# Optimization experiments

Hardware: AMD Instinct MI355X
Metric: run time of the kernel (lower is better)

## Reference

```python
import jax, jax.numpy as jnp
import numpy as np

B, T, L, F = 32, 512, 16, 128   # utterances, max frames, frame-spec width, specgram_height
H = 128                          # hidden_size1 == hidden_size2
C = 61                           # TIMIT phoneme count


def _p(key, shape, scale):
    return jax.random.normal(key, shape, jnp.float32) * scale


def setup_inputs() -> dict:
    key = jax.random.key(0)
    ks = jax.random.split(key, 32)
    s = 1.0 / np.sqrt(H)
    inp = {}
    inp["x"] = jax.random.normal(ks[0], (B, T, L, F), jnp.float32)
    inp["lengths"] = jax.random.randint(ks[1], (B,), T // 2, T + 1, jnp.int32)
    i = 2
    # rnn1: tanh-RNN, 2 layers, bidirectional (layer0 in=F, layer1 in=2H); dir axis 0
    for name, din in (("r1l0", F), ("r1l1", 2 * H)):
        inp[name + "_Wih"] = _p(ks[i], (2, H, din), s); i += 1
        inp[name + "_Whh"] = _p(ks[i], (2, H, H), s); i += 1
        inp[name + "_bih"] = _p(ks[i], (2, H), s); i += 1
        inp[name + "_bhh"] = _p(ks[i], (2, H), s); i += 1
    # rnn2: GRU, 2 layers, bidirectional (in=2H for both layers); gates packed r,z,n
    for name in ("g0", "g1"):
        inp[name + "_Wih"] = _p(ks[i], (2, 3 * H, 2 * H), s); i += 1
        inp[name + "_Whh"] = _p(ks[i], (2, 3 * H, H), s); i += 1
        inp[name + "_bih"] = _p(ks[i], (2, 3 * H), s); i += 1
        inp[name + "_bhh"] = _p(ks[i], (2, 3 * H), s); i += 1
    inp["fc_W"] = _p(ks[i], (C, 2 * H), s); i += 1
    inp["fc_b"] = _p(ks[i], (C,), s)
    return inp


def _rnn_bidir(x, Wih, Whh, bih, bhh):
    # x: (N, S, din) -> (N, S, 2H); PyTorch nn.RNN(tanh), bidirectional
    outs = []
    for d in range(2):
        xw = jnp.einsum('bli,hi->blh', x, Wih[d]) + bih[d]
        W, b = Whh[d], bhh[d]
        def step(h, xt):
            h = jnp.tanh(xt + h @ W.T + b)
            return h, h
        h0 = jnp.zeros((x.shape[0], W.shape[0]), x.dtype)
        _, ys = jax.lax.scan(step, h0, jnp.swapaxes(xw, 0, 1), reverse=(d == 1))
        outs.append(jnp.swapaxes(ys, 0, 1))
    return jnp.concatenate(outs, -1)


def _gru_bidir(x, Wih, Whh, bih, bhh):
    # x: (N, S, din) -> (N, S, 2H); PyTorch nn.GRU, bidirectional
    outs = []
    for d in range(2):
        xw = jnp.einsum('bli,hi->blh', x, Wih[d]) + bih[d]  # (N, S, 3H)
        W, b = Whh[d], bhh[d]
        def step(h, xt):
            g = h @ W.T + b
            xr, xz, xn = jnp.split(xt, 3, -1)
            gr, gz, gn = jnp.split(g, 3, -1)
            r = jax.nn.sigmoid(xr + gr)
            z = jax.nn.sigmoid(xz + gz)
            n = jnp.tanh(xn + r * gn)
            h = (1.0 - z) * n + z * h
            return h, h
        h0 = jnp.zeros((x.shape[0], W.shape[1]), x.dtype)
        _, ys = jax.lax.scan(step, h0, jnp.swapaxes(xw, 0, 1), reverse=(d == 1))
        outs.append(jnp.swapaxes(ys, 0, 1))
    return jnp.concatenate(outs, -1)


def reference(x, lengths,
              r1l0_Wih, r1l0_Whh, r1l0_bih, r1l0_bhh,
              r1l1_Wih, r1l1_Whh, r1l1_bih, r1l1_bhh,
              g0_Wih, g0_Whh, g0_bih, g0_bhh,
              g1_Wih, g1_Whh, g1_bih, g1_bhh,
              fc_W, fc_b):
    b, t, l, f = x.shape
    # per-sample rnn1 loop == one batched pass over all B*T frames (eval mode: no dropout)
    o = _rnn_bidir(x.reshape(b * t, l, f), r1l0_Wih, r1l0_Whh, r1l0_bih, r1l0_bhh)
    o = _rnn_bidir(o, r1l1_Wih, r1l1_Whh, r1l1_bih, r1l1_bhh)
    o = o[:, -1, :].reshape(b, t, 2 * H)       # last inner timestep per frame
    o = _gru_bidir(o, g0_Wih, g0_Whh, g0_bih, g0_bhh)
    o = _gru_bidir(o, g1_Wih, g1_Whh, g1_bih, g1_bhh)
    logits = o @ fc_W.T + fc_b                  # (B, T, C)
    mask = jnp.arange(t)[None, :] < lengths[:, None]
    # ragged scatter: concat first lengths[i] timesteps of each sample
    return logits.reshape(b * t, -1)[mask.reshape(-1)]
```

## Files before the change

### kernel.cpp

```cpp
#include <hip/hip_runtime.h>
#include <hip/hip_bf16.h>

#define B_ 32
#define T_ 512
#define L_ 16
#define F_ 128
#define H_ 128
#define C_ 61
#define NF_ (B_*T_)
#define CH_ 4096

typedef unsigned int u32;
typedef unsigned short u16;
typedef __attribute__((ext_vector_type(8))) short s16x8;
typedef __attribute__((ext_vector_type(4))) float f32x4;

__device__ __forceinline__ float bflo(u32 v){ return __uint_as_float(v << 16); }
__device__ __forceinline__ float bfhi(u32 v){ return __uint_as_float(v & 0xffff0000u); }
__device__ __forceinline__ u16 f2bf(float f){
  u32 u = __float_as_uint(f);
  u += 0x7fffu + ((u >> 16) & 1u);
  return (u16)(u >> 16);
}
__device__ __forceinline__ u32 pack2(float a, float b){
  return (u32)f2bf(a) | ((u32)f2bf(b) << 16);
}
__device__ __forceinline__ float fast_tanh(float x){
  float e = __expf(2.f*x);
  return 1.f - 2.f*__builtin_amdgcn_rcpf(e + 1.f);
}
__device__ __forceinline__ float fast_sigmoid(float x){
  return __builtin_amdgcn_rcpf(1.f + __expf(-x));
}
__device__ __forceinline__ f32x4 mfma16(s16x8 a, s16x8 b, f32x4 c){
  return __builtin_amdgcn_mfma_f32_16x16x32_bf16(a, b, c, 0, 0, 0);
}
__device__ __forceinline__ s16x8 packfrag(const float* p){
  const float4 a = *(const float4*)p;
  const float4 b = *(const float4*)(p+4);
  union { s16x8 v; u32 w[4]; } f;
  f.w[0]=pack2(a.x,a.y); f.w[1]=pack2(a.z,a.w);
  f.w[2]=pack2(b.x,b.y); f.w[3]=pack2(b.z,b.w);
  return f.v;
}

__global__ __launch_bounds__(256) void l0_mfma(
    const float* __restrict__ x,
    const float* __restrict__ Wih,
    const float* __restrict__ Whh,
    const float* __restrict__ bih,
    const float* __restrict__ bhh,
    u16* __restrict__ out)
{
  __shared__ __align__(16) u16 Hb[2][32][136];
  __shared__ __align__(16) u16 Xb[2][32][136];
  const int t = threadIdx.x;
  const int lane = t & 63, wv = t >> 6;
  const int l15 = lane & 15, kg = lane >> 4;
  const int dir = blockIdx.y;
  const int f0 = blockIdx.x * 32;
  s16x8 wih[2][4], whh[2][4];
  {
    const float* Wid = Wih + dir*16384;
    const float* Whd = Whh + dir*16384;
    #pragma unroll
    for (int nt = 0; nt < 2; nt++){
      const int u = wv*32 + nt*16 + l15;
      #pragma unroll
      for (int kc = 0; kc < 4; kc++){
        const int k = kc*32 + kg*8;
        wih[nt][kc] = packfrag(&Wid[u*128 + k]);
        whh[nt][kc] = packfrag(&Whd[u*128 + k]);
      }
    }
  }
  float bv[2];
  bv[0] = bih[dir*128 + wv*32 + l15]      + bhh[dir*128 + wv*32 + l15];
  bv[1] = bih[dir*128 + wv*32 + 16 + l15] + bhh[dir*128 + wv*32 + 16 + l15];
  const int sr = t >> 3, sc = (t & 7) * 16;
  {
    *(uint4*)&Hb[0][sr][sc]   = make_uint4(0,0,0,0);
    *(uint4*)&Hb[0][sr][sc+8] = make_uint4(0,0,0,0);
    const int s0 = dir ? 15 : 0;
    const float4* xp = (const float4*)&x[(size_t)(f0+sr)*2048 + s0*128 + sc];
    const float4 v0 = xp[0], v1 = xp[1], v2 = xp[2], v3 = xp[3];
    *(uint4*)&Xb[0][sr][sc]   = make_uint4(pack2(v0.x,v0.y),pack2(v0.z,v0.w),
                                           pack2(v1.x,v1.y),pack2(v1.z,v1.w));
    *(uint4*)&Xb[0][sr][sc+8] = make_uint4(pack2(v2.x,v2.y),pack2(v2.z,v2.w),
                                           pack2(v3.x,v3.y),pack2(v3.z,v3.w));
  }
  __syncthreads();
  int cur = 0;
  for (int st = 0; st < 16; st++){
    const int s = dir ? (15-st) : st;
    float4 p0,p1,p2,p3;
    if (st < 15){
      const int sn = dir ? (14-st) : (st+1);
      const float4* xp = (const float4*)&x[(size_t)(f0+sr)*2048 + sn*128 + sc];
      p0 = xp[0]; p1 = xp[1]; p2 = xp[2]; p3 = xp[3];
    }
    f32x4 acc00 = {0.f,0.f,0.f,0.f}, acc01 = acc00, acc10 = acc00, acc11 = acc00;
    #pragma unroll
    for (int kc = 0; kc < 4; kc++){
      const int ko = kc*32 + kg*8;
      const s16x8 ax0 = *(const s16x8*)&Xb[cur][l15][ko];
      const s16x8 ax1 = *(const s16x8*)&Xb[cur][16+l15][ko];
      const s16x8 ah0 = *(const s16x8*)&Hb[cur][l15][ko];
      const s16x8 ah1 = *(const s16x8*)&Hb[cur][16+l15][ko];
      acc00 = mfma16(ax0, wih[0][kc], acc00);
      acc01 = mfma16(ax0, wih[1][kc], acc01);
      acc10 = mfma16(ax1, wih[0][kc], acc10);
      acc11 = mfma16(ax1, wih[1][kc], acc11);
      acc00 = mfma16(ah0, whh[0][kc], acc00);
      acc01 = mfma16(ah0, whh[1][kc], acc01);
      acc10 = mfma16(ah1, whh[0][kc], acc10);
      acc11 = mfma16(ah1, whh[1][kc], acc11);
    }
    const int u0 = wv*32 + l15, u1 = wv*32 + 16 + l15;
    u16* op = out + (size_t)f0*4096 + s*256 + dir*128;
    #pragma unroll
    for (int r = 0; r < 4; r++){
      const int m0r = kg*4 + r, m1r = 16 + kg*4 + r;
      u16 h00 = f2bf(fast_tanh(acc00[r] + bv[0]));
      u16 h01 = f2bf(fast_tanh(acc01[r] + bv[1]));
      u16 h10 = f2bf(fast_tanh(acc10[r] + bv[0]));
      u16 h11 = f2bf(fast_tanh(acc11[r] + bv[1]));
      Hb[cur^1][m0r][u0] = h00;
      Hb[cur^1][m0r][u1] = h01;
      Hb[cur^1][m1r][u0] = h10;
      Hb[cur^1][m1r][u1] = h11;
      op[(size_t)m0r*4096 + u0] = h00;
      op[(size_t)m0r*4096 + u1] = h01;
      op[(size_t)m1r*4096 + u0] = h10;
      op[(size_t)m1r*4096 + u1] = h11;
    }
    if (st < 15){
      *(uint4*)&Xb[cur^1][sr][sc]   = make_uint4(pack2(p0.x,p0.y),pack2(p0.z,p0.w),
                                                 pack2(p1.x,p1.y),pack2(p1.z,p1.w));
      *(uint4*)&Xb[cur^1][sr][sc+8] = make_uint4(pack2(p2.x,p2.y),pack2(p2.z,p2.w),
                                                 pack2(p3.x,p3.y),pack2(p3.z,p3.w));
    }
    __syncthreads();
    cur ^= 1;
  }
}

__global__ __launch_bounds__(256) void l1f_mfma(
    const u16* __restrict__ U,
    const float* __restrict__ Wih,
    const float* __restrict__ Whh,
    const float* __restrict__ bih,
    const float* __restrict__ bhh,
    u16* __restrict__ out)
{
  __shared__ __align__(16) u16 Hb[2][32][136];
  __shared__ __align__(16) u16 Xb[2][32][264];
  const int t = threadIdx.x;
  const int lane = t & 63, wv = t >> 6;
  const int l15 = lane & 15, kg = lane >> 4;
  const int f0 = blockIdx.x * 32;
  s16x8 wih[2][8], whh[2][4];
  {
    #pragma unroll
    for (int nt = 0; nt < 2; nt++){
      const int u = wv*32 + nt*16 + l15;
      #pragma unroll
      for (int kc = 0; kc < 8; kc++)
        wih[nt][kc] = packfrag(&Wih[u*256 + kc*32 + kg*8]);
      #pragma unroll
      for (int kc = 0; kc < 4; kc++)
        whh[nt][kc] = packfrag(&Whh[u*128 + kc*32 + kg*8]);
    }
  }
  float bv[2];
  bv[0] = bih[wv*32 + l15]      + bhh[wv*32 + l15];
  bv[1] = bih[wv*32 + 16 + l15] + bhh[wv*32 + 16 + l15];
  const int sr = t >> 3, sc = (t & 7) * 32;
  {
    *(uint4*)&Hb[0][sr][(t&7)*16]   = make_uint4(0,0,0,0);
    *(uint4*)&Hb[0][sr][(t&7)*16+8] = make_uint4(0,0,0,0);
    const uint4* up = (const uint4*)&U[(size_t)(f0+sr)*4096 + 0*256 + sc];
    uint4 c0 = up[0], c1 = up[1], c2 = up[2], c3 = up[3];
    *(uint4*)&Xb[0][sr][sc]    = c0;
    *(uint4*)&Xb[0][sr][sc+8]  = c1;
    *(uint4*)&Xb[0][sr][sc+16] = c2;
    *(uint4*)&Xb[0][sr][sc+24] = c3;
  }
  __syncthreads();
  int cur = 0;
  for (int st = 0; st < 16; st++){
    uint4 c0,c1,c2,c3;
    if (st < 15){
      const uint4* up = (const uint4*)&U[(size_t)(f0+sr)*4096 + (st+1)*256 + sc];
      c0 = up[0]; c1 = up[1]; c2 = up[2]; c3 = up[3];
    }
    f32x4 acc00 = {0.f,0.f,0.f,0.f}, acc01 = acc00, acc10 = acc00, acc11 = acc00;
    #pragma unroll
    for (int kc = 0; kc < 8; kc++){
      const int ko = kc*32 + kg*8;
      const s16x8 ax0 = *(const s16x8*)&Xb[cur][l15][ko];
      const s16x8 ax1 = *(const s16x8*)&Xb[cur][16+l15][ko];
      acc00 = mfma16(ax0, wih[0][kc], acc00);
      acc01 = mfma16(ax0, wih[1][kc], acc01);
      acc10 = mfma16(ax1, wih[0][kc], acc10);
      acc11 = mfma16(ax1, wih[1][kc], acc11);
    }
    #pragma unroll
    for (int kc = 0; kc < 4; kc++){
      const int ko = kc*32 + kg*8;
      const s16x8 ah0 = *(const s16x8*)&Hb[cur][l15][ko];
      const s16x8 ah1 = *(const s16x8*)&Hb[cur][16+l15][ko];
      acc00 = mfma16(ah0, whh[0][kc], acc00);
      acc01 = mfma16(ah0, whh[1][kc], acc01);
      acc10 = mfma16(ah1, whh[0][kc], acc10);
      acc11 = mfma16(ah1, whh[1][kc], acc11);
    }
    const int u0 = wv*32 + l15, u1 = wv*32 + 16 + l15;
    #pragma unroll
    for (int r = 0; r < 4; r++){
      const int m0r = kg*4 + r, m1r = 16 + kg*4 + r;
      const u16 h00 = f2bf(fast_tanh(acc00[r] + bv[0]));
      const u16 h01 = f2bf(fast_tanh(acc01[r] + bv[1]));
      const u16 h10 = f2bf(fast_tanh(acc10[r] + bv[0]));
      const u16 h11 = f2bf(fast_tanh(acc11[r] + bv[1]));
      Hb[cur^1][m0r][u0] = h00;
      Hb[cur^1][m0r][u1] = h01;
      Hb[cur^1][m1r][u0] = h10;
      Hb[cur^1][m1r][u1] = h11;
      if (st == 15){
        out[(size_t)(f0+m0r)*256 + u0] = h00;
        out[(size_t)(f0+m0r)*256 + u1] = h01;
        out[(size_t)(f0+m1r)*256 + u0] = h10;
        out[(size_t)(f0+m1r)*256 + u1] = h11;
      }
    }
    if (st < 15){
      *(uint4*)&Xb[cur^1][sr][sc]    = c0;
      *(uint4*)&Xb[cur^1][sr][sc+8]  = c1;
      *(uint4*)&Xb[cur^1][sr][sc+16] = c2;
      *(uint4*)&Xb[cur^1][sr][sc+24] = c3;
    }
    __syncthreads();
    cur ^= 1;
  }
}

__global__ __launch_bounds__(256) void mfma_gemm(
    const u16* __restrict__ A, int lda,
    const u16* __restrict__ Wb, int K,
    const float* __restrict__ bias,
    float* __restrict__ Cf, u16* __restrict__ Cb, int ldc, int act)
{
  const int t = threadIdx.x;
  const int lane = t & 63, wv = t >> 6;
  const int l15 = lane & 15, kg = lane >> 4;
  const int n0 = blockIdx.x * 32;
  const int m0 = blockIdx.y * 64 + wv*16;
  const u16* Ap = A + (size_t)(m0 + l15)*lda + kg*8;
  const u16* W0 = Wb + (size_t)(n0 + l15)*K + kg*8;
  const u16* W1 = Wb + (size_t)(n0 + 16 + l15)*K + kg*8;
  f32x4 acc0 = {0.f,0.f,0.f,0.f}, acc1 = acc0;
  #pragma unroll 4
  for (int kc = 0; kc < K/32; kc++){
    const s16x8 a  = *(const s16x8*)(Ap + kc*32);
    const s16x8 b0 = *(const s16x8*)(W0 + kc*32);
    const s16x8 b1 = *(const s16x8*)(W1 + kc*32);
    acc0 = mfma16(a, b0, acc0);
    acc1 = mfma16(a, b1, acc1);
  }
  const int col0 = n0 + l15, col1 = n0 + 16 + l15;
  const float bv0 = bias[col0], bv1 = bias[col1];
  #pragma unroll
  for (int r = 0; r < 4; r++){
    const int row = m0 + kg*4 + r;
    float v0 = acc0[r] + bv0, v1 = acc1[r] + bv1;
    if (act){ v0 = fast_tanh(v0); v1 = fast_tanh(v1); }
    if (Cf){
      Cf[(size_t)row*ldc + col0] = v0;
      Cf[(size_t)row*ldc + col1] = v1;
    } else {
      Cb[(size_t)row*ldc + col0] = f2bf(v0);
      Cb[(size_t)row*ldc + col1] = f2bf(v1);
    }
  }
}

__global__ __launch_bounds__(256) void gemm_xw(
    const u16* __restrict__ A, int lda,
    const u16* __restrict__ Wb, int K,
    const float* __restrict__ bias,
    float* __restrict__ xwT)
{
  const int t = threadIdx.x;
  const int lane = t & 63, wv = t >> 6;
  const int l15 = lane & 15, kg = lane >> 4;
  const int n0 = blockIdx.x * 32;
  const int m0 = blockIdx.y * 64 + wv*16;
  const u16* Ap = A + (size_t)(m0 + l15)*lda + kg*8;
  const u16* W0 = Wb + (size_t)(n0 + l15)*K + kg*8;
  const u16* W1 = Wb + (size_t)(n0 + 16 + l15)*K + kg*8;
  f32x4 acc0 = {0.f,0.f,0.f,0.f}, acc1 = acc0;
  #pragma unroll 4
  for (int kc = 0; kc < K/32; kc++){
    const s16x8 a  = *(const s16x8*)(Ap + kc*32);
    const s16x8 b0 = *(const s16x8*)(W0 + kc*32);
    const s16x8 b1 = *(const s16x8*)(W1 + kc*32);
    acc0 = mfma16(a, b0, acc0);
    acc1 = mfma16(a, b1, acc1);
  }
  const int col0 = n0 + l15, col1 = n0 + 16 + l15;
  const float bv0 = bias[col0], bv1 = bias[col1];
  const int d0 = col0 >= 384, d1 = col1 >= 384;
  const int c0 = col0 - d0*384, c1 = col1 - d1*384;
  #pragma unroll
  for (int r = 0; r < 4; r++){
    const int row = m0 + kg*4 + r;
    const int b = row >> 9, tt = row & 511;
    xwT[((size_t)(d0*512 + tt)*32 + b)*384 + c0] = acc0[r] + bv0;
    xwT[((size_t)(d1*512 + tt)*32 + b)*384 + c1] = acc1[r] + bv1;
  }
}

__global__ __launch_bounds__(256) void prep_kernel(
    const float* __restrict__ g0W, const float* __restrict__ g1W,
    const float* __restrict__ r1Wih,
    const float* __restrict__ r1bih, const float* __restrict__ r1bhh,
    u16* __restrict__ g0o, u16* __restrict__ g1o, u16* __restrict__ r1o,
    float* __restrict__ bo)
{
  const int i = blockIdx.x*256 + threadIdx.x;
  if (i < 196608){ g0o[i] = f2bf(g0W[i]); g1o[i] = f2bf(g1W[i]); }
  if (i < 32768)   r1o[i] = f2bf(r1Wih[32768 + i]);
  if (i < 128)     bo[i]  = r1bih[128+i] + r1bhh[128+i];
}

__global__ __launch_bounds__(512) void gru_mfma(
    const float* __restrict__ xwT,
    const float* __restrict__ Whh,
    const float* __restrict__ bhh,
    u16* __restrict__ hout)
{
  __shared__ __align__(16) u16 h_lds[2][16][136];
  const int t = threadIdx.x;
  const int lane = t & 63, wv = t >> 6;
  const int l15 = lane & 15, kg = lane >> 4;
  const int dir = blockIdx.x & 1, half = blockIdx.x >> 1;
  const int b0 = half*16;
  const int us = wv*16;
  s16x8 wb[3][4];
  {
    const float* Wd = Whh + (size_t)dir*49152;
    #pragma unroll
    for (int g = 0; g < 3; g++)
      #pragma unroll
      for (int kc = 0; kc < 4; kc++)
        wb[g][kc] = packfrag(&Wd[(size_t)(g*128 + us + l15)*128 + kc*32 + kg*8]);
  }
  float bh[3];
  #pragma unroll
  for (int g = 0; g < 3; g++) bh[g] = bhh[dir*384 + g*128 + us + l15];
  if (t < 272) ((uint4*)&h_lds[0][0][0])[t] = make_uint4(0,0,0,0);
  float hreg[4] = {0.f,0.f,0.f,0.f};
  const float* xwb = xwT + (size_t)dir*512*32*384;
  float px0[4][3], px1[4][3];
#define LOADX(TT, PX)                                                        \
  _Pragma("unroll")                                                          \
  for (int r = 0; r < 4; r++){                                               \
    const float* xp = xwb + ((size_t)(TT)*32 + b0 + kg*4 + r)*384 + us + l15;\
    PX[r][0] = xp[0]; PX[r][1] = xp[128]; PX[r][2] = xp[256];                \
  }
  LOADX(dir ? 511 : 0, px0);
  LOADX(dir ? 510 : 1, px1);
  __syncthreads();
  int cur = 0;

#define GSTEP(TI, PX)                                                        \
  {                                                                          \
    const int tt = dir ? (511-(TI)) : (TI);                                  \
    s16x8 af[4];                                                             \
    _Pragma("unroll")                                                        \
    for (int kc = 0; kc < 4; kc++)                                           \
      af[kc] = *(const s16x8*)&h_lds[cur][l15][kc*32 + kg*8];                \
    f32x4 a0 = {0.f,0.f,0.f,0.f}, a1 = a0, a2 = a0;                          \
    _Pragma("unroll")                                                        \
    for (int kc = 0; kc < 4; kc++){                                          \
      a0 = mfma16(af[kc], wb[0][kc], a0);                                    \
      a1 = mfma16(af[kc], wb[1][kc], a1);                                    \
      a2 = mfma16(af[kc], wb[2][kc], a2);                                    \
    }                                                                        \
    _Pragma("unroll")                                                        \
    for (int r = 0; r < 4; r++){                                             \
      const float rr = fast_sigmoid(PX[r][0] + a0[r] + bh[0]);               \
      const float zz = fast_sigmoid(PX[r][1] + a1[r] + bh[1]);               \
      const float nn = fast_tanh(PX[r][2] + rr*(a2[r] + bh[2]));             \
      const float hn = (1.f - zz)*nn + zz*hreg[r];                           \
      hreg[r] = hn;                                                          \
      const u16 hb = f2bf(hn);                                               \
      h_lds[cur^1][kg*4+r][us + l15] = hb;                                   \
      hout[((size_t)(b0+kg*4+r)*512 + tt)*256 + dir*128 + us + l15] = hb;    \
    }                                                                        \
    { int ti2 = (TI)+2; ti2 = ti2 > 511 ? 511 : ti2;                         \
      const int tn = dir ? (511-ti2) : ti2;                                  \
      LOADX(tn, PX); }                                                       \
    __syncthreads();                                                         \
    cur ^= 1;                                                                \
  }

  for (int ti = 0; ti < 512; ti += 2){
    GSTEP(ti,   px0);
    GSTEP(ti+1, px1);
  }
#undef GSTEP
#undef LOADX
}

__global__ void prefix_kernel(const int* __restrict__ lengths, int* __restrict__ pre){
  if (threadIdx.x == 0 && blockIdx.x == 0){
    int run = 0;
    for (int b = 0; b < 32; b++){ pre[b] = run; run += lengths[b]; }
  }
}

__global__ __launch_bounds__(256) void fc_kernel(
    const u16* __restrict__ A,
    const float* __restrict__ W,
    const float* __restrict__ bias,
    const int* __restrict__ lengths,
    const int* __restrict__ pre,
    float* __restrict__ out)
{
  __shared__ __align__(16) float4 Wl[64][61];
  __shared__ __align__(16) float  Al[64][256];
  const int t = threadIdx.x;
  const int row0 = blockIdx.x * 64;
  for (int idx = t; idx < 61*64; idx += 256){
    int c = idx >> 6, k4 = idx & 63;
    Wl[k4][c] = *(const float4*)&W[(size_t)c*256 + k4*4];
  }
  {
    const u32* A32 = (const u32*)(A + (size_t)row0*256);
    for (int idx = t; idx < 8192; idx += 256){
      u32 v = A32[idx];
      int r = idx >> 7, kp = idx & 127;
      Al[r][2*kp]   = bflo(v);
      Al[r][2*kp+1] = bfhi(v);
    }
  }
  __syncthreads();
  const int c = t & 63;
  const int rbase = t >> 6;
  if (c < 61){
    const float bv = bias[c];
    for (int rr = rbase; rr < 64; rr += 4){
      float s0=0,s1=0,s2=0,s3=0;
      const float4* Ap = (const float4*)&Al[rr][0];
      #pragma unroll
      for (int k4 = 0; k4 < 64; k4++){
        const float4 w = Wl[k4][c];
        const float4 a = Ap[k4];
        s0 = fmaf(w.x, a.x, s0);
        s1 = fmaf(w.y, a.y, s1);
        s2 = fmaf(w.z, a.z, s2);
        s3 = fmaf(w.w, a.w, s3);
      }
      const int n = row0 + rr;
      const int b = n >> 9, tt = n & 511;
      if (tt < lengths[b])
        out[(size_t)(pre[b] + tt)*61 + c] = bv + s0+s1+s2+s3;
    }
  }
}

extern "C" void kernel_launch(void* const* d_in, const int* in_sizes, int n_in,
                              void* d_out, int out_size, void* d_ws, size_t ws_size,
                              hipStream_t stream)
{
  const float* x     = (const float*)d_in[0];
  const int*   lens  = (const int*)d_in[1];
  const float* r0Wih = (const float*)d_in[2];
  const float* r0Whh = (const float*)d_in[3];
  const float* r0bih = (const float*)d_in[4];
  const float* r0bhh = (const float*)d_in[5];
  const float* r1Wih = (const float*)d_in[6];
  const float* r1Whh = (const float*)d_in[7];
  const float* r1bih = (const float*)d_in[8];
  const float* r1bhh = (const float*)d_in[9];
  const float* g0Wih = (const float*)d_in[10];
  const float* g0Whh = (const float*)d_in[11];
  const float* g0bih = (const float*)d_in[12];
  const float* g0bhh = (const float*)d_in[13];
  const float* g1Wih = (const float*)d_in[14];
  const float* g1Whh = (const float*)d_in[15];
  const float* g1bih = (const float*)d_in[16];
  const float* g1bhh = (const float*)d_in[17];
  const float* fcW   = (const float*)d_in[18];
  const float* fcb   = (const float*)d_in[19];
  float* out = (float*)d_out;

  char* ws = (char*)d_ws;
  u16*   l0buf = (u16*)(ws);
  float* xwbuf = (float*)(ws);
  u16*   g0out = (u16*)(ws + 50331648);
  u16*   g0Wb  = (u16*)(ws + 58720256);
  u16*   g1Wb  = (u16*)(ws + 58720256 + 393216);
  u16*   r1Wb  = (u16*)(ws + 58720256 + 786432);
  float* biasb = (float*)(ws + 58720256 + 851968);
  u16*   g1out = (u16*)(ws + 58720256);
  u16*   rnn1  = (u16*)(ws + 67108864);
  int*   pre   = (int*)(ws + 75497472);

  prep_kernel<<<768, 256, 0, stream>>>(g0Wih, g1Wih, r1Wih, r1bih, r1bhh,
                                       g0Wb, g1Wb, r1Wb, biasb);
  for (int c = 0; c < NF_/CH_; c++){
    l0_mfma<<<dim3(CH_/32, 2), 256, 0, stream>>>(
        x + (size_t)c*CH_*2048, r0Wih, r0Whh, r0bih, r0bhh, l0buf);
    l1f_mfma<<<dim3(CH_/32), 256, 0, stream>>>(
        l0buf, r1Wih, r1Whh, r1bih, r1bhh, rnn1 + (size_t)c*CH_*256);
    mfma_gemm<<<dim3(128/32, CH_/64), 256, 0, stream>>>(
        l0buf + 15*256, 4096, r1Wb, 256, biasb,
        (float*)nullptr, rnn1 + (size_t)c*CH_*256 + 128, 256, 1);
  }
  gemm_xw<<<dim3(768/32, NF_/64), 256, 0, stream>>>(
      rnn1, 256, g0Wb, 256, g0bih, xwbuf);
  gru_mfma<<<4, 512, 0, stream>>>(xwbuf, g0Whh, g0bhh, g0out);
  gemm_xw<<<dim3(768/32, NF_/64), 256, 0, stream>>>(
      g0out, 256, g1Wb, 256, g1bih, xwbuf);
  gru_mfma<<<4, 512, 0, stream>>>(xwbuf, g1Whh, g1bhh, g1out);
  prefix_kernel<<<1, 64, 0, stream>>>(lens, pre);
  fc_kernel<<<NF_/64, 256, 0, stream>>>(g1out, fcW, fcb, lens, pre, out);
}
```

Baseline: 1.184 ms.

## Relayout GRU input projections for vector loads; halve l1f frames per block

The gemm_xw epilogue now writes the input projection in a layout permuted to match the GRU kernel's per-lane fragment ownership. Each GRU lane can then fetch its r/z/n values for a timestep with three contiguous 16-byte loads through a strided pointer, replacing twelve scattered scalar loads and per-step index arithmetic. Separately, l1f_mfma processes 16 frames per block instead of 32, doubling the grid to improve occupancy and latency hiding on the recurrent layer, though each block gets less MFMA work per barrier. The gemm store becomes more scattered, and the new index math is intricate.

```diff
diff --git a/kernel.cpp b/kernel.cpp
--- a/kernel.cpp
+++ b/kernel.cpp
@@ -153,12 +153,12 @@
     const float* __restrict__ bhh,
     u16* __restrict__ out)
 {
-  __shared__ __align__(16) u16 Hb[2][32][136];
-  __shared__ __align__(16) u16 Xb[2][32][264];
+  __shared__ __align__(16) u16 Hb[2][16][136];
+  __shared__ __align__(16) u16 Xb[2][16][264];
   const int t = threadIdx.x;
   const int lane = t & 63, wv = t >> 6;
   const int l15 = lane & 15, kg = lane >> 4;
-  const int f0 = blockIdx.x * 32;
+  const int f0 = blockIdx.x * 16;
   s16x8 wih[2][8], whh[2][4];
   {
     #pragma unroll
@@ -175,70 +175,52 @@
   float bv[2];
   bv[0] = bih[wv*32 + l15]      + bhh[wv*32 + l15];
   bv[1] = bih[wv*32 + 16 + l15] + bhh[wv*32 + 16 + l15];
-  const int sr = t >> 3, sc = (t & 7) * 32;
+  const int sr = t >> 4, scu = (t & 15) * 16;
+  for (int idx = t; idx < 272; idx += 256)
+    ((uint4*)&Hb[0][0][0])[idx] = make_uint4(0,0,0,0);
   {
-    *(uint4*)&Hb[0][sr][(t&7)*16]   = make_uint4(0,0,0,0);
-    *(uint4*)&Hb[0][sr][(t&7)*16+8] = make_uint4(0,0,0,0);
-    const uint4* up = (const uint4*)&U[(size_t)(f0+sr)*4096 + 0*256 + sc];
-    uint4 c0 = up[0], c1 = up[1], c2 = up[2], c3 = up[3];
-    *(uint4*)&Xb[0][sr][sc]    = c0;
-    *(uint4*)&Xb[0][sr][sc+8]  = c1;
-    *(uint4*)&Xb[0][sr][sc+16] = c2;
-    *(uint4*)&Xb[0][sr][sc+24] = c3;
+    const uint4* up = (const uint4*)&U[(size_t)(f0+sr)*4096 + scu];
+    uint4 c0 = up[0], c1 = up[1];
+    *(uint4*)&Xb[0][sr][scu]   = c0;
+    *(uint4*)&Xb[0][sr][scu+8] = c1;
   }
   __syncthreads();
   int cur = 0;
   for (int st = 0; st < 16; st++){
-    uint4 c0,c1,c2,c3;
+    uint4 c0,c1;
     if (st < 15){
-      const uint4* up = (const uint4*)&U[(size_t)(f0+sr)*4096 + (st+1)*256 + sc];
-      c0 = up[0]; c1 = up[1]; c2 = up[2]; c3 = up[3];
-    }
-    f32x4 acc00 = {0.f,0.f,0.f,0.f}, acc01 = acc00, acc10 = acc00, acc11 = acc00;
+      const uint4* up = (const uint4*)&U[(size_t)(f0+sr)*4096 + (st+1)*256 + scu];
+      c0 = up[0]; c1 = up[1];
+    }
+    f32x4 acc0 = {0.f,0.f,0.f,0.f}, acc1 = acc0;
     #pragma unroll
     for (int kc = 0; kc < 8; kc++){
-      const int ko = kc*32 + kg*8;
-      const s16x8 ax0 = *(const s16x8*)&Xb[cur][l15][ko];
-      const s16x8 ax1 = *(const s16x8*)&Xb[cur][16+l15][ko];
-      acc00 = mfma16(ax0, wih[0][kc], acc00);
-      acc01 = mfma16(ax0, wih[1][kc], acc01);
-      acc10 = mfma16(ax1, wih[0][kc], acc10);
-      acc11 = mfma16(ax1, wih[1][kc], acc11);
+      const s16x8 ax = *(const s16x8*)&Xb[cur][l15][kc*32 + kg*8];
+      acc0 = mfma16(ax, wih[0][kc], acc0);
+      acc1 = mfma16(ax, wih[1][kc], acc1);
     }
     #pragma unroll
     for (int kc = 0; kc < 4; kc++){
-      const int ko = kc*32 + kg*8;
-      const s16x8 ah0 = *(const s16x8*)&Hb[cur][l15][ko];
-      const s16x8 ah1 = *(const s16x8*)&Hb[cur][16+l15][ko];
-      acc00 = mfma16(ah0, whh[0][kc], acc00);
-      acc01 = mfma16(ah0, whh[1][kc], acc01);
-      acc10 = mfma16(ah1, whh[0][kc], acc10);
-      acc11 = mfma16(ah1, whh[1][kc], acc11);
+      const s16x8 ah = *(const s16x8*)&Hb[cur][l15][kc*32 + kg*8];
+      acc0 = mfma16(ah, whh[0][kc], acc0);
+      acc1 = mfma16(ah, whh[1][kc], acc1);
     }
     const int u0 = wv*32 + l15, u1 = wv*32 + 16 + l15;
     #pragma unroll
     for (int r = 0; r < 4; r++){
-      const int m0r = kg*4 + r, m1r = 16 + kg*4 + r;
-      const u16 h00 = f2bf(fast_tanh(acc00[r] + bv[0]));
-      const u16 h01 = f2bf(fast_tanh(acc01[r] + bv[1]));
-      const u16 h10 = f2bf(fast_tanh(acc10[r] + bv[0]));
-      const u16 h11 = f2bf(fast_tanh(acc11[r] + bv[1]));
-      Hb[cur^1][m0r][u0] = h00;
-      Hb[cur^1][m0r][u1] = h01;
-      Hb[cur^1][m1r][u0] = h10;
-      Hb[cur^1][m1r][u1] = h11;
+      const int m = kg*4 + r;
+      const u16 h0 = f2bf(fast_tanh(acc0[r] + bv[0]));
+      const u16 h1 = f2bf(fast_tanh(acc1[r] + bv[1]));
+      Hb[cur^1][m][u0] = h0;
+      Hb[cur^1][m][u1] = h1;
       if (st == 15){
-        out[(size_t)(f0+m0r)*256 + u0] = h00;
-        out[(size_t)(f0+m0r)*256 + u1] = h01;
-        out[(size_t)(f0+m1r)*256 + u0] = h10;
-        out[(size_t)(f0+m1r)*256 + u1] = h11;
+        out[(size_t)(f0+m)*256 + u0] = h0;
+        out[(size_t)(f0+m)*256 + u1] = h1;
       }
     }
     if (st < 15){
-      *(uint4*)&Xb[cur^1][sr][sc]    = c0;
-      *(uint4*)&Xb[cur^1][sr][sc+8]  = c1;
-      *(uint4*)&Xb[cur^1][sr][sc+16] = c2;
-      *(uint4*)&Xb[cur^1][sr][sc+24] = c3;
+      *(uint4*)&Xb[cur^1][sr][scu]   = c0;
+      *(uint4*)&Xb[cur^1][sr][scu+8] = c1;
     }
     __syncthreads();
     cur ^= 1;
@@ -310,14 +292,20 @@
   }
   const int col0 = n0 + l15, col1 = n0 + 16 + l15;
   const float bv0 = bias[col0], bv1 = bias[col1];
+  const int row0 = m0 + kg*4;
+  const int b   = row0 >> 9;
+  const int tt0 = row0 & 511;
+  const int half = b >> 4, kg2 = (b & 15) >> 2, r2 = b & 3;
   const int d0 = col0 >= 384, d1 = col1 >= 384;
-  const int c0 = col0 - d0*384, c1 = col1 - d1*384;
+  const int cc0 = col0 - d0*384, cc1 = col1 - d1*384;
+  const size_t i0 = (((((size_t)d0*512 + tt0)*2 + half)*8 + (cc0>>7? 0:0) + ((cc0&127)>>4))*4 + kg2)*192
+                    + (size_t)(cc0&15)*12 + (cc0>>7)*4 + r2;
+  const size_t i1 = (((((size_t)d1*512 + tt0)*2 + half)*8 + ((cc1&127)>>4))*4 + kg2)*192
+                    + (size_t)(cc1&15)*12 + (cc1>>7)*4 + r2;
   #pragma unroll
   for (int r = 0; r < 4; r++){
-    const int row = m0 + kg*4 + r;
-    const int b = row >> 9, tt = row & 511;
-    xwT[((size_t)(d0*512 + tt)*32 + b)*384 + c0] = acc0[r] + bv0;
-    xwT[((size_t)(d1*512 + tt)*32 + b)*384 + c1] = acc1[r] + bv1;
+    xwT[i0 + (size_t)r*12288] = acc0[r] + bv0;
+    xwT[i1 + (size_t)r*12288] = acc1[r] + bv1;
   }
 }
 
@@ -356,62 +344,73 @@
       for (int kc = 0; kc < 4; kc++)
         wb[g][kc] = packfrag(&Wd[(size_t)(g*128 + us + l15)*128 + kc*32 + kg*8]);
   }
-  float bh[3];
-  #pragma unroll
-  for (int g = 0; g < 3; g++) bh[g] = bhh[dir*384 + g*128 + us + l15];
+  const float bh0 = bhh[dir*384 + us + l15];
+  const float bh1 = bhh[dir*384 + 128 + us + l15];
+  const float bh2 = bhh[dir*384 + 256 + us + l15];
   if (t < 272) ((uint4*)&h_lds[0][0][0])[t] = make_uint4(0,0,0,0);
   float hreg[4] = {0.f,0.f,0.f,0.f};
-  const float* xwb = xwT + (size_t)dir*512*32*384;
-  float px0[4][3], px1[4][3];
-#define LOADX(TT, PX)                                                        \
-  _Pragma("unroll")                                                          \
-  for (int r = 0; r < 4; r++){                                               \
-    const float* xp = xwb + ((size_t)(TT)*32 + b0 + kg*4 + r)*384 + us + l15;\
-    PX[r][0] = xp[0]; PX[r][1] = xp[128]; PX[r][2] = xp[256];                \
-  }
-  LOADX(dir ? 511 : 0, px0);
-  LOADX(dir ? 510 : 1, px1);
+  const long tstep = dir ? -49152 : 49152;
+  const char* xb = (const char*)xwT
+      + ((size_t)dir*512 + (dir ? 511 : 0))*49152
+      + (size_t)((((half*8 + wv)*4 + kg)*16 + l15)*12)*4;
+  f32x4 px0[3], px1[3];
+  px0[0] = *(const f32x4*)(xb); px0[1] = *(const f32x4*)(xb+16); px0[2] = *(const f32x4*)(xb+32);
+  xb += tstep;
+  px1[0] = *(const f32x4*)(xb); px1[1] = *(const f32x4*)(xb+16); px1[2] = *(const f32x4*)(xb+32);
+  xb += tstep;
+  const int hstep = dir ? -256 : 256;
+  int hoff[4];
+  #pragma unroll
+  for (int r = 0; r < 4; r++)
+    hoff[r] = ((b0 + kg*4 + r)*512 + (dir ? 511 : 0))*256 + dir*128 + us + l15;
   __syncthreads();
   int cur = 0;
 
-#define GSTEP(TI, PX)                                                        \
-  {                                                                          \
-    const int tt = dir ? (511-(TI)) : (TI);                                  \
-    s16x8 af[4];                                                             \
-    _Pragma("unroll")                                                        \
-    for (int kc = 0; kc < 4; kc++)                                           \
-      af[kc] = *(const s16x8*)&h_lds[cur][l15][kc*32 + kg*8];                \
-    f32x4 a0 = {0.f,0.f,0.f,0.f}, a1 = a0, a2 = a0;                          \
-    _Pragma("unroll")                                                        \
-    for (int kc = 0; kc < 4; kc++){                                          \
-      a0 = mfma16(af[kc], wb[0][kc], a0);                                    \
-      a1 = mfma16(af[kc], wb[1][kc], a1);                                    \
-      a2 = mfma16(af[kc], wb[2][kc], a2);                                    \
-    }                                                                        \
-    _Pragma("unroll")                                                        \
-    for (int r = 0; r < 4; r++){                                             \
-      const float rr = fast_sigmoid(PX[r][0] + a0[r] + bh[0]);               \
-      const float zz = fast_sigmoid(PX[r][1] + a1[r] + bh[1]);               \
-      const float nn = fast_tanh(PX[r][2] + rr*(a2[r] + bh[2]));             \
-      const float hn = (1.f - zz)*nn + zz*hreg[r];                           \
-      hreg[r] = hn;                                                          \
-      const u16 hb = f2bf(hn);                                               \
-      h_lds[cur^1][kg*4+r][us + l15] = hb;                                   \
-      hout[((size_t)(b0+kg*4+r)*512 + tt)*256 + dir*128 + us + l15] = hb;    \
-    }                                                                        \
-    { int ti2 = (TI)+2; ti2 = ti2 > 511 ? 511 : ti2;                         \
-      const int tn = dir ? (511-ti2) : ti2;                                  \
-      LOADX(tn, PX); }                                                       \
-    __syncthreads();                                                         \
-    cur ^= 1;                                                                \
+#define GSTEP(PX)                                                           \
+  {                                                                         \
+    const s16x8 af0 = *(const s16x8*)&h_lds[cur][l15][kg*8];                \
+    const s16x8 af1 = *(const s16x8*)&h_lds[cur][l15][32+kg*8];             \
+    const s16x8 af2 = *(const s16x8*)&h_lds[cur][l15][64+kg*8];             \
+    const s16x8 af3 = *(const s16x8*)&h_lds[cur][l15][96+kg*8];             \
+    f32x4 a0 = {0.f,0.f,0.f,0.f}, a1 = a0, a2 = a0;                         \
+    a0 = mfma16(af0, wb[0][0], a0);                                         \
+    a1 = mfma16(af0, wb[1][0], a1);                                         \
+    a2 = mfma16(af0, wb[2][0], a2);                                         \
+    a0 = mfma16(af1, wb[0][1], a0);                                         \
+    a1 = mfma16(af1, wb[1][1], a1);                                         \
+    a2 = mfma16(af1, wb[2][1], a2);                                         \
+    a0 = mfma16(af2, wb[0][2], a0);                                         \
+    a1 = mfma16(af2, wb[1][2], a1);                                         \
+    a2 = mfma16(af2, wb[2][2], a2);                                         \
+    a0 = mfma16(af3, wb[0][3], a0);                                         \
+    a1 = mfma16(af3, wb[1][3], a1);                                         \
+    a2 = mfma16(af3, wb[2][3], a2);                                         \
+    const f32x4 n0 = *(const f32x4*)(xb);                                   \
+    const f32x4 n1 = *(const f32x4*)(xb+16);                                \
+    const f32x4 n2 = *(const f32x4*)(xb+32);                                \
+    xb += tstep;                                                            \
+    _Pragma("unroll")                                                       \
+    for (int r = 0; r < 4; r++){                                            \
+      const float rr = fast_sigmoid(PX[0][r] + a0[r] + bh0);                \
+      const float zz = fast_sigmoid(PX[1][r] + a1[r] + bh1);                \
+      const float nn = fast_tanh(PX[2][r] + rr*(a2[r] + bh2));              \
+      const float hn = fmaf(zz, hreg[r]-nn, nn);                            \
+      hreg[r] = hn;                                                         \
+      const u16 hb = f2bf(hn);                                              \
+      h_lds[cur^1][kg*4+r][us+l15] = hb;                                    \
+      hout[hoff[r]] = hb;                                                   \
+      hoff[r] += hstep;                                                     \
+    }                                                                       \
+    PX[0] = n0; PX[1] = n1; PX[2] = n2;                                     \
+    __syncthreads();                                                        \
+    cur ^= 1;                                                               \
   }
 
   for (int ti = 0; ti < 512; ti += 2){
-    GSTEP(ti,   px0);
-    GSTEP(ti+1, px1);
+    GSTEP(px0);
+    GSTEP(px1);
   }
 #undef GSTEP
-#undef LOADX
 }
 
 __global__ void prefix_kernel(const int* __restrict__ lengths, int* __restrict__ pre){
@@ -514,7 +513,7 @@
   for (int c = 0; c < NF_/CH_; c++){
     l0_mfma<<<dim3(CH_/32, 2), 256, 0, stream>>>(
         x + (size_t)c*CH_*2048, r0Wih, r0Whh, r0bih, r0bhh, l0buf);
-    l1f_mfma<<<dim3(CH_/32), 256, 0, stream>>>(
+    l1f_mfma<<<dim3(CH_/16), 256, 0, stream>>>(
         l0buf, r1Wih, r1Whh, r1bih, r1bhh, rnn1 + (size_t)c*CH_*256);
     mfma_gemm<<<dim3(128/32, CH_/64), 256, 0, stream>>>(
         l0buf + 15*256, 4096, r1Wb, 256, biasb,
```

Result: no change. 1.163 ms (-1.8%).
